# Kernel optimization log

Hardware: AMD Instinct MI355X
Metric: run time of the kernel (lower is better)

Reference implementation:

```python
import jax, jax.numpy as jnp
import numpy as np

H = 8              # n_heads
N_PER_GRAPH = 64   # nodes per graph (equal-sized graphs)


def setup_inputs() -> dict:
    key = jax.random.key(0)
    ks = jax.random.split(key, 5)
    total, D = 65536, 512
    x = jax.random.normal(ks[0], (total, D), dtype=jnp.float32)
    batch = jnp.arange(total, dtype=jnp.int64) // N_PER_GRAPH  # sorted graph ids
    s = 1.0 / np.sqrt(D).astype(np.float32)
    # nn.MultiheadAttention packed in-proj (xavier-ish uniform) + zero bias
    in_proj_w = jax.random.uniform(ks[1], (3 * D, D), jnp.float32, -s, s)
    in_proj_b = jnp.zeros((3 * D,), jnp.float32)
    out_proj_w = jax.random.uniform(ks[2], (D, D), jnp.float32, -s, s)
    out_proj_b = jnp.zeros((D,), jnp.float32)
    gate_w = jax.random.uniform(ks[3], (1, D), jnp.float32, -s, s)
    gate_b = jnp.zeros((1,), jnp.float32)
    return {"x": x, "batch": batch, "in_proj_w": in_proj_w, "in_proj_b": in_proj_b,
            "out_proj_w": out_proj_w, "out_proj_b": out_proj_b,
            "gate_w": gate_w, "gate_b": gate_b}


def reference(x, batch, in_proj_w, in_proj_b, out_proj_w, out_proj_b, gate_w, gate_b):
    total, D = x.shape
    G = total // N_PER_GRAPH
    hd = D // H
    xg = x.reshape(G, N_PER_GRAPH, D)                       # [G, N, D]
    # packed qkv projection (torch: x @ in_proj_w.T + in_proj_b)
    qkv = jnp.einsum('gnd,ed->gne', xg, in_proj_w) + in_proj_b
    q, k, v = jnp.split(qkv, 3, axis=-1)
    def to_heads(t):
        return t.reshape(G, N_PER_GRAPH, H, hd).transpose(0, 2, 1, 3)  # [G, H, N, hd]
    q, k, v = to_heads(q), to_heads(k), to_heads(v)
    scores = jnp.einsum('ghnd,ghmd->ghnm', q, k) * (1.0 / np.sqrt(hd))
    attn = jax.nn.softmax(scores, axis=-1)
    ctx = jnp.einsum('ghnm,ghmd->ghnd', attn, v)
    ctx = ctx.transpose(0, 2, 1, 3).reshape(G, N_PER_GRAPH, D)
    attn_out = jnp.einsum('gnd,ed->gne', ctx, out_proj_w) + out_proj_b  # [G, N, D]
    gates = jax.nn.sigmoid(jnp.einsum('gnd,od->gno', attn_out, gate_w) + gate_b)
    return (attn_out * gates).sum(axis=1)                   # [G, D]
```

## Files before the change

### kernel.cpp

```cpp
#include <hip/hip_runtime.h>
#include <stdint.h>


typedef __attribute__((ext_vector_type(8))) short short8;
typedef __attribute__((ext_vector_type(4))) float f32x4;

#define D_ 512

#define WQKV_OFF   0u
#define WO_OFF     1572864u
#define UPART_OFF  2097152u
#define U_OFF      2129920u
#define C0_OFF     2131968u
#define SG_OFF     2132032u
#define WCTX_OFF   2136128u

__device__ __forceinline__ unsigned short f2bf(float f) {
    union { float f; unsigned int u; } t; t.f = f;
    unsigned int u = t.u;
    return (unsigned short)((u + 0x7FFFu + ((u >> 16) & 1u)) >> 16);
}
__device__ __forceinline__ unsigned pack2(float a, float b) {
    return (unsigned)f2bf(a) | ((unsigned)f2bf(b) << 16);
}
__device__ __forceinline__ int swz(int r, int m) {
    return r*64 + ((((m >> 3) ^ (r & 7)) << 3) | (m & 7));
}

__global__ __launch_bounds__(256)
void convert_and_u(const float* __restrict__ wqkv, const float* __restrict__ wo,
                   const float* __restrict__ gw,
                   unsigned short* __restrict__ wbf, float* __restrict__ upart) {
    const int b = blockIdx.x;
    const int t = threadIdx.x;
    if (b < 1024) {
        const int i4 = b * 256 + t;
        float4 v;
        if (i4 < 196608) v = *(const float4*)(wqkv + (size_t)i4 * 4);
        else             v = *(const float4*)(wo   + (size_t)(i4 - 196608) * 4);
        uint2 p; p.x = pack2(v.x, v.y); p.y = pack2(v.z, v.w);
        *(uint2*)(wbf + (size_t)i4 * 4) = p;
    } else {
        const int bb = b - 1024;
        float a0 = 0.f, a1 = 0.f;
        #pragma unroll 4
        for (int e = bb * 32; e < bb * 32 + 32; ++e) {
            const float ge = gw[e];
            a0 += wo[(size_t)e * 512 + t]       * ge;
            a1 += wo[(size_t)e * 512 + t + 256] * ge;
        }
        upart[bb * 512 + t] = a0; upart[bb * 512 + t + 256] = a1;
    }
}

__global__ __launch_bounds__(256)
void finalize_u(const float* __restrict__ upart, const float* __restrict__ bo,
                const float* __restrict__ gw, const float* __restrict__ gb,
                float* __restrict__ u, float* __restrict__ c0) {
    const int t = threadIdx.x;
    float s0 = 0.f, s1 = 0.f;
    #pragma unroll
    for (int b = 0; b < 16; ++b) { s0 += upart[b*512 + t]; s1 += upart[b*512 + t + 256]; }
    u[t] = s0; u[t + 256] = s1;
    __shared__ float rb[256];
    rb[t] = bo[t] * gw[t] + bo[t + 256] * gw[t + 256];
    __syncthreads();
    for (int s = 128; s > 0; s >>= 1) { if (t < s) rb[t] += rb[t + s]; __syncthreads(); }
    if (t == 0) c0[0] = rb[0] + gb[0];
}

union U8 { unsigned u[4]; short8 s; };

__global__ __launch_bounds__(512, 4)
void attn_ctx_kernel(const float* __restrict__ x,
                     const unsigned short* __restrict__ wqkv,
                     const float* __restrict__ bqkv,
                     const float* __restrict__ u,
                     const float* __restrict__ c0,
                     unsigned short* __restrict__ wctx_ws,
                     float* __restrict__ sumgate)
{
    __shared__ unsigned short xs[64][520];
    __shared__ float logitp[8][64];
    __shared__ float gatev[64];

    const int g    = blockIdx.x;
    const int tid  = threadIdx.x;
    const int w    = tid >> 6;
    const int lane = tid & 63;
    const int l15  = lane & 15;
    const int quad = lane >> 4;

    #pragma unroll
    for (int i = 0; i < 16; ++i) {
        int idx = tid + i * 512;
        int row = idx >> 7;
        int c4  = idx & 127;
        float4 v = *(const float4*)(x + ((size_t)(g*64 + row))*512 + c4*4);
        uint2 p; p.x = pack2(v.x, v.y); p.y = pack2(v.z, v.w);
        *(uint2*)(&xs[row][c4*4]) = p;
    }
    __syncthreads();

    const int h = w;

    U8 qA[4][2], kB[4][2];
    #pragma unroll
    for (int dt = 0; dt < 4; ++dt) {
        f32x4 aq[4], ak[4];
        #pragma unroll
        for (int nt = 0; nt < 4; ++nt) {
            aq[nt] = (f32x4){0.f,0.f,0.f,0.f};
            ak[nt] = (f32x4){0.f,0.f,0.f,0.f};
        }
        const unsigned short* wq = wqkv + (size_t)(       h*64 + dt*16 + l15) * 512;
        const unsigned short* wk = wqkv + (size_t)(512 +  h*64 + dt*16 + l15) * 512;
        #pragma unroll 4
        for (int ks = 0; ks < 16; ++ks) {
            const int col = ks*32 + quad*8;
            short8 a0 = *(const short8*)(wq + col);
            short8 a1 = *(const short8*)(wk + col);
            #pragma unroll
            for (int nt = 0; nt < 4; ++nt) {
                short8 b = *(const short8*)(&xs[nt*16 + l15][col]);
                aq[nt] = __builtin_amdgcn_mfma_f32_16x16x32_bf16(a0, b, aq[nt], 0,0,0);
                ak[nt] = __builtin_amdgcn_mfma_f32_16x16x32_bf16(a1, b, ak[nt], 0,0,0);
            }
        }
        float bq[4], bk2[4];
        #pragma unroll
        for (int r = 0; r < 4; ++r) {
            bq[r]  = bqkv[       h*64 + dt*16 + quad*4 + r];
            bk2[r] = bqkv[512 +  h*64 + dt*16 + quad*4 + r];
        }
        const bool take = ((quad >> 1) == (dt & 1));
        const int  ks2  = dt >> 1;
        #pragma unroll
        for (int nt = 0; nt < 4; ++nt) {
            unsigned q01 = pack2(aq[nt][0]+bq[0],  aq[nt][1]+bq[1]);
            unsigned q23 = pack2(aq[nt][2]+bq[2],  aq[nt][3]+bq[3]);
            unsigned k01 = pack2(ak[nt][0]+bk2[0], ak[nt][1]+bk2[1]);
            unsigned k23 = pack2(ak[nt][2]+bk2[2], ak[nt][3]+bk2[3]);
            #pragma unroll
            for (int j = 0; j < 4; ++j) {
                int srcl = ((quad & 1)*2 + (j >> 1))*16 + l15;
                unsigned tq = (unsigned)__shfl((int)((j & 1) ? q23 : q01), srcl);
                unsigned tk = (unsigned)__shfl((int)((j & 1) ? k23 : k01), srcl);
                if (take) { qA[nt][ks2].u[j] = tq; kB[nt][ks2].u[j] = tk; }
            }
        }
    }

    f32x4 sacc[4][4];
    #pragma unroll
    for (int a = 0; a < 4; ++a)
        #pragma unroll
        for (int b = 0; b < 4; ++b) sacc[a][b] = (f32x4){0.f,0.f,0.f,0.f};
    #pragma unroll
    for (int ks2 = 0; ks2 < 2; ++ks2)
        #pragma unroll
        for (int a = 0; a < 4; ++a)
            #pragma unroll
            for (int b = 0; b < 4; ++b)
                sacc[a][b] = __builtin_amdgcn_mfma_f32_16x16x32_bf16(
                                 qA[a][ks2].s, kB[b][ks2].s, sacc[a][b], 0,0,0);

    #pragma unroll
    for (int a = 0; a < 4; ++a) {
        #pragma unroll
        for (int r = 0; r < 4; ++r) {
            float m0 = -1e30f;
            #pragma unroll
            for (int b = 0; b < 4; ++b) { sacc[a][b][r] *= 0.125f; m0 = fmaxf(m0, sacc[a][b][r]); }
            m0 = fmaxf(m0, __shfl_xor(m0, 1));
            m0 = fmaxf(m0, __shfl_xor(m0, 2));
            m0 = fmaxf(m0, __shfl_xor(m0, 4));
            m0 = fmaxf(m0, __shfl_xor(m0, 8));
            float s = 0.f;
            #pragma unroll
            for (int b = 0; b < 4; ++b) { float e = __expf(sacc[a][b][r] - m0); sacc[a][b][r] = e; s += e; }
            s += __shfl_xor(s, 1); s += __shfl_xor(s, 2); s += __shfl_xor(s, 4); s += __shfl_xor(s, 8);
            float inv = 1.0f / s;
            #pragma unroll
            for (int b = 0; b < 4; ++b) sacc[a][b][r] *= inv;
        }
    }
    unsigned ppk[4][4][2];
    #pragma unroll
    for (int a = 0; a < 4; ++a)
        #pragma unroll
        for (int b = 0; b < 4; ++b) {
            ppk[a][b][0] = pack2(sacc[a][b][0], sacc[a][b][1]);
            ppk[a][b][1] = pack2(sacc[a][b][2], sacc[a][b][3]);
        }

    unsigned avpk[4][4][2];
    #pragma unroll
    for (int dt = 0; dt < 4; ++dt) {
        f32x4 av[4];
        #pragma unroll
        for (int nt = 0; nt < 4; ++nt) av[nt] = (f32x4){0.f,0.f,0.f,0.f};
        const unsigned short* wv = wqkv + (size_t)(1024 + h*64 + dt*16 + l15) * 512;
        #pragma unroll 4
        for (int ks = 0; ks < 16; ++ks) {
            const int col = ks*32 + quad*8;
            short8 a2 = *(const short8*)(wv + col);
            #pragma unroll
            for (int nt = 0; nt < 4; ++nt) {
                short8 b = *(const short8*)(&xs[nt*16 + l15][col]);
                av[nt] = __builtin_amdgcn_mfma_f32_16x16x32_bf16(a2, b, av[nt], 0,0,0);
            }
        }
        float bv2[4];
        #pragma unroll
        for (int r = 0; r < 4; ++r) bv2[r] = bqkv[1024 + h*64 + dt*16 + quad*4 + r];
        #pragma unroll
        for (int nt = 0; nt < 4; ++nt) {
            avpk[dt][nt][0] = pack2(av[nt][0]+bv2[0], av[nt][1]+bv2[1]);
            avpk[dt][nt][1] = pack2(av[nt][2]+bv2[2], av[nt][3]+bv2[3]);
        }
    }

    __syncthreads();
    unsigned short* S = ((unsigned short*)xs) + w*4096;

    #pragma unroll
    for (int dt = 0; dt < 4; ++dt)
        #pragma unroll
        for (int nt = 0; nt < 4; ++nt)
            #pragma unroll
            for (int p = 0; p < 2; ++p) {
                unsigned uu = avpk[dt][nt][p];
                int d = dt*16 + quad*4 + 2*p;
                int m = nt*16 + l15;
                S[swz(d,   m)] = (unsigned short)(uu & 0xFFFFu);
                S[swz(d+1, m)] = (unsigned short)(uu >> 16);
            }
    U8 vA[4][2];
    #pragma unroll
    for (int dtile = 0; dtile < 4; ++dtile)
        #pragma unroll
        for (int ks2 = 0; ks2 < 2; ++ks2) {
            int row = dtile*16 + l15;
            int ch  = (ks2*4 + quad) ^ (row & 7);
            vA[dtile][ks2].s = *(const short8*)(S + row*64 + ch*8);
        }
    #pragma unroll
    for (int a = 0; a < 4; ++a)
        #pragma unroll
        for (int b = 0; b < 4; ++b)
            #pragma unroll
            for (int p = 0; p < 2; ++p) {
                unsigned uu = ppk[a][b][p];
                int n = a*16 + quad*4 + 2*p;
                int m = b*16 + l15;
                S[swz(n,   m)] = (unsigned short)(uu & 0xFFFFu);
                S[swz(n+1, m)] = (unsigned short)(uu >> 16);
            }
    U8 pB[4][2];
    #pragma unroll
    for (int a = 0; a < 4; ++a)
        #pragma unroll
        for (int ks2 = 0; ks2 < 2; ++ks2) {
            int row = a*16 + l15;
            int ch  = (ks2*4 + quad) ^ (row & 7);
            pB[a][ks2].s = *(const short8*)(S + row*64 + ch*8);
        }

    f32x4 cacc[4][4];
    #pragma unroll
    for (int dtile = 0; dtile < 4; ++dtile)
        #pragma unroll
        for (int a = 0; a < 4; ++a) cacc[dtile][a] = (f32x4){0.f,0.f,0.f,0.f};
    #pragma unroll
    for (int ks2 = 0; ks2 < 2; ++ks2)
        #pragma unroll
        for (int dtile = 0; dtile < 4; ++dtile)
            #pragma unroll
            for (int a = 0; a < 4; ++a)
                cacc[dtile][a] = __builtin_amdgcn_mfma_f32_16x16x32_bf16(
                                     vA[dtile][ks2].s, pB[a][ks2].s, cacc[dtile][a], 0,0,0);

    {
        float uv[4][4];
        #pragma unroll
        for (int dtile = 0; dtile < 4; ++dtile)
            #pragma unroll
            for (int r = 0; r < 4; ++r)
                uv[dtile][r] = u[h*64 + dtile*16 + quad*4 + r];
        #pragma unroll
        for (int a = 0; a < 4; ++a) {
            float s = 0.f;
            #pragma unroll
            for (int dtile = 0; dtile < 4; ++dtile)
                #pragma unroll
                for (int r = 0; r < 4; ++r)
                    s += cacc[dtile][a][r] * uv[dtile][r];
            s += __shfl_xor(s, 16); s += __shfl_xor(s, 32);
            if (quad == 0) logitp[w][a*16 + l15] = s;
        }
    }
    __syncthreads();

    if (tid < 64) {
        float lg = c0[0];
        #pragma unroll
        for (int ww = 0; ww < 8; ++ww) lg += logitp[ww][tid];
        float gt = 1.0f / (1.0f + __expf(-lg));
        gatev[tid] = gt;
        float s = gt;
        s += __shfl_xor(s, 1);  s += __shfl_xor(s, 2);  s += __shfl_xor(s, 4);
        s += __shfl_xor(s, 8);  s += __shfl_xor(s, 16); s += __shfl_xor(s, 32);
        if (tid == 0) sumgate[g] = s;
    }
    __syncthreads();

    {
        float gv[4];
        #pragma unroll
        for (int a = 0; a < 4; ++a) gv[a] = gatev[a*16 + l15];
        #pragma unroll
        for (int dtile = 0; dtile < 4; ++dtile) {
            float sr[4];
            #pragma unroll
            for (int r = 0; r < 4; ++r) {
                float s = cacc[dtile][0][r]*gv[0] + cacc[dtile][1][r]*gv[1]
                        + cacc[dtile][2][r]*gv[2] + cacc[dtile][3][r]*gv[3];
                s += __shfl_xor(s, 1); s += __shfl_xor(s, 2);
                s += __shfl_xor(s, 4); s += __shfl_xor(s, 8);
                sr[r] = s;
            }
            if (l15 == 0) {
                uint2 pk; pk.x = pack2(sr[0], sr[1]); pk.y = pack2(sr[2], sr[3]);
                *(uint2*)(wctx_ws + (size_t)g*512 + h*64 + dtile*16 + quad*4) = pk;
            }
        }
    }
}

__global__ __launch_bounds__(256, 4)
void outproj_kernel(const unsigned short* __restrict__ wo_bf,
                    const unsigned short* __restrict__ wctx_bf,
                    const float* __restrict__ bo,
                    const float* __restrict__ sumgate,
                    float* __restrict__ out)
{
    const int tid  = threadIdx.x;
    const int w    = tid >> 6;
    const int lane = tid & 63;
    const int l15  = lane & 15;
    const int quad = lane >> 4;
    const int g0   = blockIdx.x * 32;

    f32x4 oac[8][2];
    #pragma unroll
    for (int et = 0; et < 8; ++et)
        #pragma unroll
        for (int mt = 0; mt < 2; ++mt)
            oac[et][mt] = (f32x4){0.f,0.f,0.f,0.f};

    #pragma unroll 4
    for (int ks = 0; ks < 16; ++ks) {
        const int col = ks*32 + quad*8;
        short8 a0 = *(const short8*)(wctx_bf + (size_t)(g0 + l15)*D_      + col);
        short8 a1 = *(const short8*)(wctx_bf + (size_t)(g0 + 16 + l15)*D_ + col);
        #pragma unroll
        for (int et = 0; et < 8; ++et) {
            short8 b = *(const short8*)(wo_bf + (size_t)(w*128 + et*16 + l15)*D_ + col);
            oac[et][0] = __builtin_amdgcn_mfma_f32_16x16x32_bf16(a0, b, oac[et][0], 0,0,0);
            oac[et][1] = __builtin_amdgcn_mfma_f32_16x16x32_bf16(a1, b, oac[et][1], 0,0,0);
        }
    }
    #pragma unroll
    for (int et = 0; et < 8; ++et) {
        const int e = w*128 + et*16 + l15;
        const float bov = bo[e];
        #pragma unroll
        for (int mt = 0; mt < 2; ++mt)
            #pragma unroll
            for (int r = 0; r < 4; ++r) {
                const int gg = g0 + mt*16 + quad*4 + r;
                out[(size_t)gg*D_ + e] = oac[et][mt][r] + sumgate[gg] * bov;
            }
    }
}

extern "C" void kernel_launch(void* const* d_in, const int* in_sizes, int n_in,
                              void* d_out, int out_size, void* d_ws, size_t ws_size,
                              hipStream_t stream) {
    const float* x    = (const float*)d_in[0];
    const float* wqkv = (const float*)d_in[2];
    const float* bqkv = (const float*)d_in[3];
    const float* wo   = (const float*)d_in[4];
    const float* bo   = (const float*)d_in[5];
    const float* gw   = (const float*)d_in[6];
    const float* gb   = (const float*)d_in[7];
    float* out = (float*)d_out;

    char* ws = (char*)d_ws;
    unsigned short* wqkv_bf = (unsigned short*)(ws + WQKV_OFF);
    unsigned short* wo_bf   = (unsigned short*)(ws + WO_OFF);
    float*          upart   = (float*)(ws + UPART_OFF);
    float*          u_ws    = (float*)(ws + U_OFF);
    float*          c0_ws   = (float*)(ws + C0_OFF);
    float*          sg_ws   = (float*)(ws + SG_OFF);
    unsigned short* wctx_ws = (unsigned short*)(ws + WCTX_OFF);

    const int total = in_sizes[0] / D_;
    const int G     = total / 64;

    hipLaunchKernelGGL(convert_and_u, dim3(1040), dim3(256), 0, stream,
                       wqkv, wo, gw, wqkv_bf, upart);
    hipLaunchKernelGGL(finalize_u,    dim3(1),    dim3(256), 0, stream,
                       upart, bo, gw, gb, u_ws, c0_ws);
    hipLaunchKernelGGL(attn_ctx_kernel, dim3(G),  dim3(512), 0, stream,
                       x, wqkv_bf, bqkv, u_ws, c0_ws, wctx_ws, sg_ws);
    hipLaunchKernelGGL(outproj_kernel, dim3(G/32), dim3(256), 0, stream,
                       wo_bf, wctx_ws, bo, sg_ws, out);
}
```

Measured before the change: 505.2 us.

## Fuse output projection into attention kernel and keep P/V in registers

Merges the separate out-projection GEMM into the per-graph attention kernel: each block now computes its gated context vector in shared memory and does a 512x512 matvec against bf16 Wo directly, removing the workspace round-trip and a launch. The scores and PV MFMAs are reoriented (transposed operands) so softmax probabilities and V fragments are redistributed with lane shuffles instead of swizzled LDS stores/loads. The trade-off is that every one of 1024 blocks reads the full 512 KB bf16 Wo through the cache with scalar FMAs instead of a batched MFMA GEMM, and the gated context is now kept in fp32 rather than rounded to bf16.

```diff
diff --git a/kernel.cpp b/kernel.cpp
--- a/kernel.cpp
+++ b/kernel.cpp
@@ -12,8 +12,6 @@
 #define UPART_OFF  2097152u
 #define U_OFF      2129920u
 #define C0_OFF     2131968u
-#define SG_OFF     2132032u
-#define WCTX_OFF   2136128u
 
 __device__ __forceinline__ unsigned short f2bf(float f) {
     union { float f; unsigned int u; } t; t.f = f;
@@ -23,8 +21,11 @@
 __device__ __forceinline__ unsigned pack2(float a, float b) {
     return (unsigned)f2bf(a) | ((unsigned)f2bf(b) << 16);
 }
-__device__ __forceinline__ int swz(int r, int m) {
-    return r*64 + ((((m >> 3) ^ (r & 7)) << 3) | (m & 7));
+__device__ __forceinline__ float blo(unsigned v) {
+    union { unsigned u; float f; } t; t.u = v << 16; return t.f;
+}
+__device__ __forceinline__ float bhi(unsigned v) {
+    union { unsigned u; float f; } t; t.u = v & 0xFFFF0000u; return t.f;
 }
 
 __global__ __launch_bounds__(256)
@@ -72,17 +73,19 @@
 union U8 { unsigned u[4]; short8 s; };
 
 __global__ __launch_bounds__(512, 4)
-void attn_ctx_kernel(const float* __restrict__ x,
-                     const unsigned short* __restrict__ wqkv,
-                     const float* __restrict__ bqkv,
-                     const float* __restrict__ u,
-                     const float* __restrict__ c0,
-                     unsigned short* __restrict__ wctx_ws,
-                     float* __restrict__ sumgate)
+void attn_full_kernel(const float* __restrict__ x,
+                      const unsigned short* __restrict__ wqkv,
+                      const float* __restrict__ bqkv,
+                      const unsigned short* __restrict__ wo_bf,
+                      const float* __restrict__ bo,
+                      const float* __restrict__ u,
+                      const float* __restrict__ c0,
+                      float* __restrict__ out)
 {
     __shared__ unsigned short xs[64][520];
     __shared__ float logitp[8][64];
     __shared__ float gatev[64];
+    __shared__ float sgs;
 
     const int g    = blockIdx.x;
     const int tid  = threadIdx.x;
@@ -151,154 +154,110 @@
         }
     }
 
-    f32x4 sacc[4][4];
+    U8 pA[4][2];
+    #pragma unroll
+    for (int a = 0; a < 4; ++a) {
+        f32x4 sc[4];
+        #pragma unroll
+        for (int b = 0; b < 4; ++b) sc[b] = (f32x4){0.f,0.f,0.f,0.f};
+        #pragma unroll
+        for (int ks2 = 0; ks2 < 2; ++ks2)
+            #pragma unroll
+            for (int b = 0; b < 4; ++b)
+                sc[b] = __builtin_amdgcn_mfma_f32_16x16x32_bf16(
+                            kB[b][ks2].s, qA[a][ks2].s, sc[b], 0,0,0);
+        float m0 = -1e30f;
+        #pragma unroll
+        for (int b = 0; b < 4; ++b)
+            #pragma unroll
+            for (int r = 0; r < 4; ++r) { sc[b][r] *= 0.125f; m0 = fmaxf(m0, sc[b][r]); }
+        m0 = fmaxf(m0, __shfl_xor(m0, 16));
+        m0 = fmaxf(m0, __shfl_xor(m0, 32));
+        float ssum = 0.f;
+        #pragma unroll
+        for (int b = 0; b < 4; ++b)
+            #pragma unroll
+            for (int r = 0; r < 4; ++r) { float e = __expf(sc[b][r] - m0); sc[b][r] = e; ssum += e; }
+        ssum += __shfl_xor(ssum, 16);
+        ssum += __shfl_xor(ssum, 32);
+        float inv = 1.0f / ssum;
+        unsigned pp[4][2];
+        #pragma unroll
+        for (int b = 0; b < 4; ++b) {
+            pp[b][0] = pack2(sc[b][0]*inv, sc[b][1]*inv);
+            pp[b][1] = pack2(sc[b][2]*inv, sc[b][3]*inv);
+        }
+        #pragma unroll
+        for (int ks2 = 0; ks2 < 2; ++ks2)
+            #pragma unroll
+            for (int j = 0; j < 4; ++j) {
+                int srcl = ((quad & 1)*2 + (j >> 1))*16 + l15;
+                unsigned t0 = (unsigned)__shfl((int)pp[ks2*2    ][j & 1], srcl);
+                unsigned t1 = (unsigned)__shfl((int)pp[ks2*2 + 1][j & 1], srcl);
+                pA[a][ks2].u[j] = (quad >> 1) ? t1 : t0;
+            }
+    }
+
+    f32x4 cacc[4][4];
     #pragma unroll
     for (int a = 0; a < 4; ++a)
         #pragma unroll
-        for (int b = 0; b < 4; ++b) sacc[a][b] = (f32x4){0.f,0.f,0.f,0.f};
-    #pragma unroll
-    for (int ks2 = 0; ks2 < 2; ++ks2)
-        #pragma unroll
-        for (int a = 0; a < 4; ++a)
-            #pragma unroll
-            for (int b = 0; b < 4; ++b)
-                sacc[a][b] = __builtin_amdgcn_mfma_f32_16x16x32_bf16(
-                                 qA[a][ks2].s, kB[b][ks2].s, sacc[a][b], 0,0,0);
-
-    #pragma unroll
-    for (int a = 0; a < 4; ++a) {
-        #pragma unroll
-        for (int r = 0; r < 4; ++r) {
-            float m0 = -1e30f;
-            #pragma unroll
-            for (int b = 0; b < 4; ++b) { sacc[a][b][r] *= 0.125f; m0 = fmaxf(m0, sacc[a][b][r]); }
-            m0 = fmaxf(m0, __shfl_xor(m0, 1));
-            m0 = fmaxf(m0, __shfl_xor(m0, 2));
-            m0 = fmaxf(m0, __shfl_xor(m0, 4));
-            m0 = fmaxf(m0, __shfl_xor(m0, 8));
-            float s = 0.f;
-            #pragma unroll
-            for (int b = 0; b < 4; ++b) { float e = __expf(sacc[a][b][r] - m0); sacc[a][b][r] = e; s += e; }
-            s += __shfl_xor(s, 1); s += __shfl_xor(s, 2); s += __shfl_xor(s, 4); s += __shfl_xor(s, 8);
-            float inv = 1.0f / s;
-            #pragma unroll
-            for (int b = 0; b < 4; ++b) sacc[a][b][r] *= inv;
-        }
-    }
-    unsigned ppk[4][4][2];
-    #pragma unroll
-    for (int a = 0; a < 4; ++a)
-        #pragma unroll
-        for (int b = 0; b < 4; ++b) {
-            ppk[a][b][0] = pack2(sacc[a][b][0], sacc[a][b][1]);
-            ppk[a][b][1] = pack2(sacc[a][b][2], sacc[a][b][3]);
-        }
-
-    unsigned avpk[4][4][2];
+        for (int dt = 0; dt < 4; ++dt) cacc[a][dt] = (f32x4){0.f,0.f,0.f,0.f};
     #pragma unroll
     for (int dt = 0; dt < 4; ++dt) {
         f32x4 av[4];
         #pragma unroll
-        for (int nt = 0; nt < 4; ++nt) av[nt] = (f32x4){0.f,0.f,0.f,0.f};
+        for (int mt = 0; mt < 4; ++mt) av[mt] = (f32x4){0.f,0.f,0.f,0.f};
         const unsigned short* wv = wqkv + (size_t)(1024 + h*64 + dt*16 + l15) * 512;
         #pragma unroll 4
         for (int ks = 0; ks < 16; ++ks) {
             const int col = ks*32 + quad*8;
             short8 a2 = *(const short8*)(wv + col);
             #pragma unroll
-            for (int nt = 0; nt < 4; ++nt) {
-                short8 b = *(const short8*)(&xs[nt*16 + l15][col]);
-                av[nt] = __builtin_amdgcn_mfma_f32_16x16x32_bf16(a2, b, av[nt], 0,0,0);
-            }
-        }
-        float bv2[4];
-        #pragma unroll
-        for (int r = 0; r < 4; ++r) bv2[r] = bqkv[1024 + h*64 + dt*16 + quad*4 + r];
-        #pragma unroll
-        for (int nt = 0; nt < 4; ++nt) {
-            avpk[dt][nt][0] = pack2(av[nt][0]+bv2[0], av[nt][1]+bv2[1]);
-            avpk[dt][nt][1] = pack2(av[nt][2]+bv2[2], av[nt][3]+bv2[3]);
-        }
-    }
-
-    __syncthreads();
-    unsigned short* S = ((unsigned short*)xs) + w*4096;
-
-    #pragma unroll
-    for (int dt = 0; dt < 4; ++dt)
-        #pragma unroll
-        for (int nt = 0; nt < 4; ++nt)
-            #pragma unroll
-            for (int p = 0; p < 2; ++p) {
-                unsigned uu = avpk[dt][nt][p];
-                int d = dt*16 + quad*4 + 2*p;
-                int m = nt*16 + l15;
-                S[swz(d,   m)] = (unsigned short)(uu & 0xFFFFu);
-                S[swz(d+1, m)] = (unsigned short)(uu >> 16);
-            }
-    U8 vA[4][2];
-    #pragma unroll
-    for (int dtile = 0; dtile < 4; ++dtile)
-        #pragma unroll
-        for (int ks2 = 0; ks2 < 2; ++ks2) {
-            int row = dtile*16 + l15;
-            int ch  = (ks2*4 + quad) ^ (row & 7);
-            vA[dtile][ks2].s = *(const short8*)(S + row*64 + ch*8);
-        }
-    #pragma unroll
-    for (int a = 0; a < 4; ++a)
-        #pragma unroll
-        for (int b = 0; b < 4; ++b)
-            #pragma unroll
-            for (int p = 0; p < 2; ++p) {
-                unsigned uu = ppk[a][b][p];
-                int n = a*16 + quad*4 + 2*p;
-                int m = b*16 + l15;
-                S[swz(n,   m)] = (unsigned short)(uu & 0xFFFFu);
-                S[swz(n+1, m)] = (unsigned short)(uu >> 16);
-            }
-    U8 pB[4][2];
-    #pragma unroll
-    for (int a = 0; a < 4; ++a)
-        #pragma unroll
-        for (int ks2 = 0; ks2 < 2; ++ks2) {
-            int row = a*16 + l15;
-            int ch  = (ks2*4 + quad) ^ (row & 7);
-            pB[a][ks2].s = *(const short8*)(S + row*64 + ch*8);
-        }
-
-    f32x4 cacc[4][4];
-    #pragma unroll
-    for (int dtile = 0; dtile < 4; ++dtile)
-        #pragma unroll
-        for (int a = 0; a < 4; ++a) cacc[dtile][a] = (f32x4){0.f,0.f,0.f,0.f};
-    #pragma unroll
-    for (int ks2 = 0; ks2 < 2; ++ks2)
-        #pragma unroll
-        for (int dtile = 0; dtile < 4; ++dtile)
+            for (int mt = 0; mt < 4; ++mt) {
+                short8 b = *(const short8*)(&xs[mt*16 + l15][col]);
+                av[mt] = __builtin_amdgcn_mfma_f32_16x16x32_bf16(b, a2, av[mt], 0,0,0);
+            }
+        }
+        const float bv = bqkv[1024 + h*64 + dt*16 + l15];
+        unsigned vpk[4][2];
+        #pragma unroll
+        for (int mt = 0; mt < 4; ++mt) {
+            vpk[mt][0] = pack2(av[mt][0]+bv, av[mt][1]+bv);
+            vpk[mt][1] = pack2(av[mt][2]+bv, av[mt][3]+bv);
+        }
+        U8 vB[2];
+        #pragma unroll
+        for (int ks2 = 0; ks2 < 2; ++ks2)
+            #pragma unroll
+            for (int j = 0; j < 4; ++j) {
+                int srcl = ((quad & 1)*2 + (j >> 1))*16 + l15;
+                unsigned t0 = (unsigned)__shfl((int)vpk[ks2*2    ][j & 1], srcl);
+                unsigned t1 = (unsigned)__shfl((int)vpk[ks2*2 + 1][j & 1], srcl);
+                vB[ks2].u[j] = (quad >> 1) ? t1 : t0;
+            }
+        #pragma unroll
+        for (int ks2 = 0; ks2 < 2; ++ks2)
             #pragma unroll
             for (int a = 0; a < 4; ++a)
-                cacc[dtile][a] = __builtin_amdgcn_mfma_f32_16x16x32_bf16(
-                                     vA[dtile][ks2].s, pB[a][ks2].s, cacc[dtile][a], 0,0,0);
+                cacc[a][dt] = __builtin_amdgcn_mfma_f32_16x16x32_bf16(
+                                  pA[a][ks2].s, vB[ks2].s, cacc[a][dt], 0,0,0);
+    }
 
     {
-        float uv[4][4];
-        #pragma unroll
-        for (int dtile = 0; dtile < 4; ++dtile)
-            #pragma unroll
-            for (int r = 0; r < 4; ++r)
-                uv[dtile][r] = u[h*64 + dtile*16 + quad*4 + r];
-        #pragma unroll
-        for (int a = 0; a < 4; ++a) {
-            float s = 0.f;
-            #pragma unroll
-            for (int dtile = 0; dtile < 4; ++dtile)
-                #pragma unroll
-                for (int r = 0; r < 4; ++r)
-                    s += cacc[dtile][a][r] * uv[dtile][r];
-            s += __shfl_xor(s, 16); s += __shfl_xor(s, 32);
-            if (quad == 0) logitp[w][a*16 + l15] = s;
-        }
+        float ul[4];
+        #pragma unroll
+        for (int dt = 0; dt < 4; ++dt) ul[dt] = u[h*64 + dt*16 + l15];
+        #pragma unroll
+        for (int a = 0; a < 4; ++a)
+            #pragma unroll
+            for (int r = 0; r < 4; ++r) {
+                float s = cacc[a][0][r]*ul[0] + cacc[a][1][r]*ul[1]
+                        + cacc[a][2][r]*ul[2] + cacc[a][3][r]*ul[3];
+                s += __shfl_xor(s, 1); s += __shfl_xor(s, 2);
+                s += __shfl_xor(s, 4); s += __shfl_xor(s, 8);
+                if (l15 == 0) logitp[w][a*16 + quad*4 + r] = s;
+            }
     }
     __syncthreads();
 
@@ -311,77 +270,41 @@
         float s = gt;
         s += __shfl_xor(s, 1);  s += __shfl_xor(s, 2);  s += __shfl_xor(s, 4);
         s += __shfl_xor(s, 8);  s += __shfl_xor(s, 16); s += __shfl_xor(s, 32);
-        if (tid == 0) sumgate[g] = s;
-    }
-    __syncthreads();
-
+        if (tid == 0) sgs = s;
+    }
+    __syncthreads();
+
+    float* wctxs = (float*)&xs[0][0];
     {
-        float gv[4];
-        #pragma unroll
-        for (int a = 0; a < 4; ++a) gv[a] = gatev[a*16 + l15];
-        #pragma unroll
-        for (int dtile = 0; dtile < 4; ++dtile) {
-            float sr[4];
-            #pragma unroll
-            for (int r = 0; r < 4; ++r) {
-                float s = cacc[dtile][0][r]*gv[0] + cacc[dtile][1][r]*gv[1]
-                        + cacc[dtile][2][r]*gv[2] + cacc[dtile][3][r]*gv[3];
-                s += __shfl_xor(s, 1); s += __shfl_xor(s, 2);
-                s += __shfl_xor(s, 4); s += __shfl_xor(s, 8);
-                sr[r] = s;
-            }
-            if (l15 == 0) {
-                uint2 pk; pk.x = pack2(sr[0], sr[1]); pk.y = pack2(sr[2], sr[3]);
-                *(uint2*)(wctx_ws + (size_t)g*512 + h*64 + dtile*16 + quad*4) = pk;
-            }
-        }
-    }
-}
-
-__global__ __launch_bounds__(256, 4)
-void outproj_kernel(const unsigned short* __restrict__ wo_bf,
-                    const unsigned short* __restrict__ wctx_bf,
-                    const float* __restrict__ bo,
-                    const float* __restrict__ sumgate,
-                    float* __restrict__ out)
-{
-    const int tid  = threadIdx.x;
-    const int w    = tid >> 6;
-    const int lane = tid & 63;
-    const int l15  = lane & 15;
-    const int quad = lane >> 4;
-    const int g0   = blockIdx.x * 32;
-
-    f32x4 oac[8][2];
-    #pragma unroll
-    for (int et = 0; et < 8; ++et)
-        #pragma unroll
-        for (int mt = 0; mt < 2; ++mt)
-            oac[et][mt] = (f32x4){0.f,0.f,0.f,0.f};
-
-    #pragma unroll 4
-    for (int ks = 0; ks < 16; ++ks) {
-        const int col = ks*32 + quad*8;
-        short8 a0 = *(const short8*)(wctx_bf + (size_t)(g0 + l15)*D_      + col);
-        short8 a1 = *(const short8*)(wctx_bf + (size_t)(g0 + 16 + l15)*D_ + col);
-        #pragma unroll
-        for (int et = 0; et < 8; ++et) {
-            short8 b = *(const short8*)(wo_bf + (size_t)(w*128 + et*16 + l15)*D_ + col);
-            oac[et][0] = __builtin_amdgcn_mfma_f32_16x16x32_bf16(a0, b, oac[et][0], 0,0,0);
-            oac[et][1] = __builtin_amdgcn_mfma_f32_16x16x32_bf16(a1, b, oac[et][1], 0,0,0);
-        }
-    }
-    #pragma unroll
-    for (int et = 0; et < 8; ++et) {
-        const int e = w*128 + et*16 + l15;
-        const float bov = bo[e];
-        #pragma unroll
-        for (int mt = 0; mt < 2; ++mt)
-            #pragma unroll
-            for (int r = 0; r < 4; ++r) {
-                const int gg = g0 + mt*16 + quad*4 + r;
-                out[(size_t)gg*D_ + e] = oac[et][mt][r] + sumgate[gg] * bov;
-            }
+        float4 gv[4];
+        #pragma unroll
+        for (int a = 0; a < 4; ++a) gv[a] = *(const float4*)&gatev[a*16 + quad*4];
+        #pragma unroll
+        for (int dt = 0; dt < 4; ++dt) {
+            float s = 0.f;
+            #pragma unroll
+            for (int a = 0; a < 4; ++a) {
+                s += cacc[a][dt][0]*gv[a].x + cacc[a][dt][1]*gv[a].y
+                   + cacc[a][dt][2]*gv[a].z + cacc[a][dt][3]*gv[a].w;
+            }
+            s += __shfl_xor(s, 16); s += __shfl_xor(s, 32);
+            if (quad == 0) wctxs[h*64 + dt*16 + l15] = s;
+        }
+    }
+    __syncthreads();
+
+    {
+        const unsigned short* wr = wo_bf + (size_t)tid * 512;
+        float acc = 0.f;
+        #pragma unroll 8
+        for (int i = 0; i < 64; ++i) {
+            uint4  w4 = *(const uint4*)(wr + i*8);
+            float4 ca = *(const float4*)(wctxs + i*8);
+            float4 cb = *(const float4*)(wctxs + i*8 + 4);
+            acc += blo(w4.x)*ca.x + bhi(w4.x)*ca.y + blo(w4.y)*ca.z + bhi(w4.y)*ca.w
+                 + blo(w4.z)*cb.x + bhi(w4.z)*cb.y + blo(w4.w)*cb.z + bhi(w4.w)*cb.w;
+        }
+        out[(size_t)g*512 + tid] = acc + sgs * bo[tid];
     }
 }
 
@@ -403,8 +326,6 @@
     float*          upart   = (float*)(ws + UPART_OFF);
     float*          u_ws    = (float*)(ws + U_OFF);
     float*          c0_ws   = (float*)(ws + C0_OFF);
-    float*          sg_ws   = (float*)(ws + SG_OFF);
-    unsigned short* wctx_ws = (unsigned short*)(ws + WCTX_OFF);
 
     const int total = in_sizes[0] / D_;
     const int G     = total / 64;
@@ -413,8 +334,6 @@
                        wqkv, wo, gw, wqkv_bf, upart);
     hipLaunchKernelGGL(finalize_u,    dim3(1),    dim3(256), 0, stream,
                        upart, bo, gw, gb, u_ws, c0_ws);
-    hipLaunchKernelGGL(attn_ctx_kernel, dim3(G),  dim3(512), 0, stream,
-                       x, wqkv_bf, bqkv, u_ws, c0_ws, wctx_ws, sg_ws);
-    hipLaunchKernelGGL(outproj_kernel, dim3(G/32), dim3(256), 0, stream,
-                       wo_bf, wctx_ws, bo, sg_ws, out);
-}
+    hipLaunchKernelGGL(attn_full_kernel, dim3(G), dim3(512), 0, stream,
+                       x, wqkv_bf, bqkv, wo_bf, bo, u_ws, c0_ws, out);
+}
```

New measurement: 452.2 us. 10.5% less time.
